# Optimization experiments

Hardware: AMD Instinct MI355X
Metric: run time of the kernel (lower is better)

## Reference

```python
import jax, jax.numpy as jnp
import numpy as np

C = 128; HEADS = 8; GH = 32; GW = 32; B = 8; PD = 8  # PD = (dim//4)//4

def _conv(x, w, pad, dil=1, groups=1):
    return jax.lax.conv_general_dilated(
        x, w, (1, 1), [(pad[0], pad[0]), (pad[1], pad[1])],
        rhs_dilation=(dil, dil),
        dimension_numbers=('NCHW', 'OIHW', 'NCHW'),
        feature_group_count=groups)

def _lrelu(t):
    return jnp.where(t >= 0, t, 0.1 * t)

def _ln(t, g, b, eps=1e-5):
    m = jnp.mean(t, -1, keepdims=True)
    v = jnp.var(t, -1, keepdims=True)
    return (t - m) * jax.lax.rsqrt(v + eps) * g + b

def setup_inputs():
    rng = np.random.RandomState(0)
    f = lambda *s: jnp.asarray((rng.randn(*s) * 0.05).astype(np.float32))
    ones = lambda n: jnp.ones((n,), jnp.float32)
    zeros = lambda n: jnp.zeros((n,), jnp.float32)
    # Swin-style relative position index over the (GH, GW) group
    coords = np.stack(np.meshgrid(np.arange(GH), np.arange(GW), indexing='ij')).reshape(2, -1)
    rel = (coords[:, :, None] - coords[:, None, :]).transpose(1, 2, 0)
    rel[..., 0] += GH - 1; rel[..., 1] += GW - 1; rel[..., 0] *= 2 * GW - 1
    rel_idx = jnp.asarray(rel.sum(-1).astype(np.int32))  # [N, N]
    biases = np.stack(np.meshgrid(np.arange(1 - GH, GH), np.arange(1 - GW, GW), indexing='ij'))
    biases = jnp.asarray(biases.reshape(2, -1).T.astype(np.float32))  # [(2GH-1)*(2GW-1), 2]
    return dict(
        x=jnp.asarray(rng.rand(B, C, GH, GW).astype(np.float32)),
        conv1_w=f(C, C, 3, 3), conv2_w=f(C, C, 3, 3), conv3_w=f(C, C, 3, 3),
        convt_w=f(C, 3, 1, 1),
        rba_w=f(C, C, 3, 1), rba_b=zeros(C), rbb_w=f(C, C, 1, 3), rbb_b=zeros(C),
        pp_w=f(PD, 2), pp_b=zeros(PD),
        l1_g=ones(PD), l1_b=zeros(PD), l1_w=f(PD, PD), l1_b2=zeros(PD),
        l2_g=ones(PD), l2_b=zeros(PD), l2_w=f(PD, PD), l2_b2=zeros(PD),
        l3_g=ones(PD), l3_b=zeros(PD), l3_w=f(HEADS, PD), l3_b2=zeros(HEADS),
        qk_w=f(2 * C, C), qk_b=zeros(2 * C),
        v_w=f(C, C), v_b=zeros(C),
        proj_w=f(C, C), proj_b=zeros(C),
        fc1_w=f(C, C), fc1_b=zeros(C), fc2_w=f(C, C), fc2_b=zeros(C),
        biases=biases, rel_idx=rel_idx,
    )

def reference(x, conv1_w, conv2_w, conv3_w, convt_w, rba_w, rba_b, rbb_w, rbb_b,
              pp_w, pp_b, l1_g, l1_b, l1_w, l1_b2, l2_g, l2_b, l2_w, l2_b2,
              l3_g, l3_b, l3_w, l3_b2, qk_w, qk_b, v_w, v_b, proj_w, proj_b,
              fc1_w, fc1_b, fc2_w, fc2_b, biases, rel_idx):
    Bn, Cc, Hh, Ww = x.shape
    N = Hh * Ww
    hd = Cc // HEADS
    # FeaExtract: ResASPP (3 dilated 3x3 convs, grouped 1x1 merge) + residual
    b1 = _lrelu(_conv(x, conv1_w, (1, 1)))
    b2 = _lrelu(_conv(x, conv2_w, (3, 3), dil=3))
    b3 = _lrelu(_conv(x, conv3_w, (5, 5), dil=5))
    a = _conv(jnp.concatenate([b1, b2, b3], 1), convt_w, (0, 0), groups=Cc) + x
    # RB: (3,1) conv -> lrelu -> (1,3) conv + residual
    r = _lrelu(_conv(a, rba_w, (1, 0)) + rba_b[None, :, None, None])
    r = _conv(r, rbb_w, (0, 1)) + rbb_b[None, :, None, None]
    o0 = r + a
    # original uses in-place clamp_, so o0 is clamped before flattening
    o0 = jnp.clip(o0, 0.0, 1.0)
    E = o0.reshape(Bn, Cc, N).transpose(0, 2, 1)  # [B, N, C]
    qk = E @ qk_w.T + qk_b  # [B, N, 2C]
    q = qk[..., :Cc].reshape(Bn, N, HEADS, hd).transpose(0, 2, 1, 3)
    k = qk[..., Cc:].reshape(Bn, N, HEADS, hd).transpose(0, 2, 1, 3)
    v = (E @ v_w.T + v_b).reshape(Bn, N, HEADS, hd).transpose(0, 2, 1, 3)
    attn = jnp.einsum('bhid,bhjd->bhij', q * (hd ** -0.5), k)
    # DynamicPosBias MLP (residual=False): Linear(2,pd) -> [LN,ReLU,Linear] x2 -> LN,ReLU,Linear(pd,heads)
    p = biases @ pp_w.T + pp_b
    p = jax.nn.relu(_ln(p, l1_g, l1_b)) @ l1_w.T + l1_b2
    p = jax.nn.relu(_ln(p, l2_g, l2_b)) @ l2_w.T + l2_b2
    p = jax.nn.relu(_ln(p, l3_g, l3_b)) @ l3_w.T + l3_b2  # [L, heads]
    rpb = p[rel_idx]  # gather -> [N, N, heads]
    attn = attn + rpb.transpose(2, 0, 1)[None]
    attn = jax.nn.softmax(attn, axis=-1)
    y = jnp.einsum('bhij,bhjd->bhid', attn, v).transpose(0, 2, 1, 3).reshape(Bn, N, Cc) + E
    x_proj = y @ proj_w.T + proj_b
    h = jax.nn.gelu(x_proj @ fc1_w.T + fc1_b, approximate=False)
    return (h @ fc2_w.T + fc2_b) + y
```

## Files before the change

### kernel.cpp

```cpp
#include <hip/hip_runtime.h>
#include <hip/hip_bf16.h>

typedef __hip_bfloat16 bf16;
typedef __bf16 bf16x8 __attribute__((ext_vector_type(8)));
typedef float f32x4 __attribute__((ext_vector_type(4)));

#define Lb 3969

#define XP_F   0
#define WF_F   903168
#define WR_F   1124352
#define WG_F   1173504
#define BH_F   1222656
#define R1P_F  1222656
#define QKV_F  1222656
#define AP_F   2795520
#define YT_F   2795520
#define EB_F   3352576
#define XPT_F  3352576
#define H1T_F  0
#define RPB_F  3876864
#define FLAG_F 3908616
#define RT_F   3908624
#define VT_F   4924432

__device__ __forceinline__ float b2f(bf16 v) { return __bfloat162float(v); }
__device__ __forceinline__ bf16 f2b(float v) { return __float2bfloat16(v); }

template <typename T> __device__ __forceinline__ float ldw(const void* p, int i);
template <> __device__ __forceinline__ float ldw<bf16>(const void* p, int i) {
  return __bfloat162float(((const bf16*)p)[i]);
}
template <> __device__ __forceinline__ float ldw<float>(const void* p, int i) {
  return ((const float*)p)[i];
}
template <typename T> __device__ __forceinline__ void stw(void* p, size_t i, float v);
template <> __device__ __forceinline__ void stw<bf16>(void* p, size_t i, float v) {
  ((bf16*)p)[i] = __float2bfloat16(v);
}
template <> __device__ __forceinline__ void stw<float>(void* p, size_t i, float v) {
  ((float*)p)[i] = v;
}

__device__ __forceinline__ unsigned pkb(float a, float b) {
  bf16 x = __float2bfloat16(a), y = __float2bfloat16(b);
  unsigned short ux = *(unsigned short*)&x, uy = *(unsigned short*)&y;
  return (unsigned)ux | ((unsigned)uy << 16);
}

__device__ __forceinline__ bool detect_local(const unsigned* x) {
  int lane = threadIdx.x & 63;
  int cnt = 0;
#pragma unroll
  for (int k = 0; k < 4; ++k) {
    unsigned lo = x[lane + 64 * k] & 0xFFFFu;
    cnt += (lo >= 0x3C00u && lo < 0x3F80u) ? 1 : 0;
  }
#pragma unroll
  for (int off = 1; off < 64; off <<= 1) cnt += __shfl_xor(cnt, off);
  return cnt >= 128;
}

template <typename T>
__device__ void wprep_all_body(const void* w1, const void* w2, const void* w3,
                               const void* rba_w, const void* rbb_w,
                               const void* qk_w, const void* v_w,
                               const void* proj_w, const void* fc1_w,
                               const void* fc2_w, bf16* __restrict__ Wf,
                               bf16* __restrict__ Wr, bf16* __restrict__ Wg)
{
  int tid = blockIdx.x * 256 + threadIdx.x;
  int lane = tid & 63, li = lane & 15, quad = lane >> 4;
  if (tid < 55296) {
    int mt = (tid >> 6) & 7;
    int Kc = (tid >> 9) & 3;
    int rem = tid >> 11;
    int t = rem % 9;
    int br = rem / 9;
    const void* w = (br == 0 ? w1 : (br == 1 ? w2 : w3));
    int o = mt * 16 + li;
    int ci0 = Kc * 32 + quad * 8;
#pragma unroll
    for (int j = 0; j < 8; ++j)
      Wf[(size_t)tid * 8 + j] = f2b(ldw<T>(w, (o * 128 + ci0 + j) * 9 + t));
  } else {
    int u = tid - 55296;
    if (u < 12288) {
      int Kc = (u >> 6) & 3, mt = (u >> 8) & 7, q = u >> 11;
      const void* w = (q >= 3) ? rbb_w : rba_w;
      int t = q % 3;
#pragma unroll
      for (int j = 0; j < 8; ++j)
        Wr[(size_t)u * 8 + j] =
            f2b(ldw<T>(w, ((mt * 16 + li) * 128 + Kc * 32 + quad * 8 + j) * 3 + t));
    } else if (u < 24576) {
      int g = u - 12288;
      int Kc = (g >> 6) & 3, mtg = g >> 8;
      const void* w; int mrow; float sc = 1.f;
      if (mtg < 16)      { w = qk_w;   mrow = mtg * 16; if (mtg < 8) sc = 0.25f; }
      else if (mtg < 24) { w = v_w;    mrow = (mtg - 16) * 16; }
      else if (mtg < 32) { w = proj_w; mrow = (mtg - 24) * 16; }
      else if (mtg < 40) { w = fc1_w;  mrow = (mtg - 32) * 16; }
      else               { w = fc2_w;  mrow = (mtg - 40) * 16; }
#pragma unroll
      for (int j = 0; j < 8; ++j)
        Wg[(size_t)g * 8 + j] =
            f2b(sc * ldw<T>(w, (mrow + li) * 128 + Kc * 32 + quad * 8 + j));
    }
  }
}

__global__ __launch_bounds__(256) void wprep_all_kernel(
    const unsigned* x, const void* w1, const void* w2, const void* w3,
    const void* rba_w, const void* rbb_w, const void* qk_w, const void* v_w,
    const void* proj_w, const void* fc1_w, const void* fc2_w,
    bf16* Wf, bf16* Wr, bf16* Wg, int* flag)
{
  bool isbf = detect_local(x);
  if (blockIdx.x == 0 && threadIdx.x == 0) *flag = isbf ? 1 : 0;
  if (isbf) wprep_all_body<bf16>(w1, w2, w3, rba_w, rbb_w, qk_w, v_w, proj_w,
                                 fc1_w, fc2_w, Wf, Wr, Wg);
  else      wprep_all_body<float>(w1, w2, w3, rba_w, rbb_w, qk_w, v_w, proj_w,
                                  fc1_w, fc2_w, Wf, Wr, Wg);
}

template <typename T>
__device__ void nhwc_body(const void* x, bf16* __restrict__ xp, bf16 (*tile)[128])
{
  const int b = blockIdx.x >> 5;
  const int row = blockIdx.x & 31;
  const int t = threadIdx.x;
  const size_t bbase = (size_t)b * 42 * 42 * 128;
  const bf16x8 z = (bf16x8){};

  if (t < 160) {
    int side = t / 80;
    int off = (t % 80) * 8;
    *(bf16x8*)&xp[bbase + ((size_t)(row + 5) * 42 + side * 37) * 128 + off] = z;
  }
  {
    int zr = (row < 5) ? row : ((row >= 27) ? row + 10 : -1);
    if (zr >= 0) {
      size_t base = bbase + (size_t)zr * 42 * 128;
      for (int k = t; k < 672; k += 256) *(bf16x8*)&xp[base + k * 8] = z;
    }
  }

  {
    int ci = t >> 1, half = t & 1;
#pragma unroll
    for (int j = 0; j < 16; ++j) {
      int px = half * 16 + j;
      tile[px][ci] = f2b(ldw<T>(x, ((size_t)b * 128 + ci) * 1024 + row * 32 + px));
    }
  }
  __syncthreads();
  {
    int px = t >> 3, c0 = (t & 7) * 16;
    bf16* dst = xp + (bbase + ((size_t)(row + 5) * 42 + (px + 5)) * 128 + c0);
#pragma unroll
    for (int j = 0; j < 16; ++j) dst[j] = tile[px][c0 + j];
  }
}

__global__ __launch_bounds__(256) void nhwc_kernel(const void* x, bf16* xp,
                                                   const int* flag)
{
  __shared__ bf16 tile[32][128];
  if (*flag) nhwc_body<bf16>(x, xp, tile);
  else       nhwc_body<float>(x, xp, tile);
}

__global__ __launch_bounds__(256) void aspp2_kernel(
    const bf16* __restrict__ xp, const bf16* __restrict__ Wf,
    bf16* __restrict__ bh)
{
  const int nt_ = blockIdx.x, br = blockIdx.y >> 1, mh = blockIdx.y & 1;
  const int bb = blockIdx.z;
  const int w = threadIdx.x >> 6, lane = threadIdx.x & 63;
  const int quad = lane >> 4, li = lane & 15;
  const int d = (br == 0 ? 1 : (br == 1 ? 3 : 5));
  const int pxw = nt_ * 64 + w * 16;
  const int y = pxw >> 5, xb = pxw & 31;

  f32x4 acc[4] = {};
  const bf16* Wbase = Wf + (size_t)br * 18432 * 8 + (size_t)mh * 4 * 64 * 8;

  for (int t = 0; t < 9; ++t) {
    const int dy = (t / 3 - 1) * d, dx = (t % 3 - 1) * d;
    const bf16* Asite =
        xp + (((size_t)bb * 42 + (y + 5 + dy)) * 42 + (xb + li + 5 + dx)) * 128;
    const bf16* Wt = Wbase + (size_t)t * 2048 * 8;
#pragma unroll
    for (int Kc = 0; Kc < 4; ++Kc) {
      bf16x8 afrag = *(const bf16x8*)(Asite + Kc * 32 + quad * 8);
      const bf16* Wk = Wt + (size_t)Kc * 512 * 8 + (size_t)lane * 8;
#pragma unroll
      for (int mt = 0; mt < 4; ++mt) {
        bf16x8 wfrag = *(const bf16x8*)(Wk + (size_t)mt * 64 * 8);
        acc[mt] = __builtin_amdgcn_mfma_f32_16x16x32_bf16(afrag, wfrag, acc[mt],
                                                          0, 0, 0);
      }
    }
  }
#pragma unroll
  for (int mt = 0; mt < 4; ++mt)
#pragma unroll
    for (int r = 0; r < 4; ++r) {
      int px = pxw + quad * 4 + r;
      bh[((size_t)bb * 1024 + px) * 384 + br * 128 + (mh * 4 + mt) * 16 + li] =
          f2b(acc[mt][r]);
    }
}

template <typename T>
__device__ void merge2_body(const bf16* __restrict__ xp, const void* wt,
                            const bf16* __restrict__ bh, bf16* __restrict__ ap,
                            float* cw)
{
  const int b = blockIdx.y, px0 = blockIdx.x * 32;
  const bf16x8 z = (bf16x8){};
  if (blockIdx.x == 0) {
    size_t base = ((size_t)b * 34 + 0) * 32 * 128;
    for (int k = threadIdx.x; k < 512; k += 256) *(bf16x8*)&ap[base + k * 8] = z;
  } else if (blockIdx.x == 31) {
    size_t base = ((size_t)b * 34 + 33) * 32 * 128;
    for (int k = threadIdx.x; k < 512; k += 256) *(bf16x8*)&ap[base + k * 8] = z;
  }
  for (int i = threadIdx.x; i < 384; i += 256) cw[i] = ldw<T>(wt, i);
  __syncthreads();
  const int pxl = threadIdx.x >> 3, og = threadIdx.x & 7;
  const int px = px0 + pxl, o0 = og * 16;
  const int y = px >> 5, x = px & 31;
  const bf16* brow = bh + ((size_t)b * 1024 + px) * 384 + o0 * 3;
  const bf16* xrow = xp + (((size_t)b * 42 + y + 5) * 42 + x + 5) * 128 + o0;
  bf16* arow = ap + (((size_t)b * 34 + y + 1) * 32 + x) * 128 + o0;

  bf16 bl[48], xl[16], ol[16];
#pragma unroll
  for (int k = 0; k < 6; ++k) *(bf16x8*)&bl[k * 8] = *(const bf16x8*)&brow[k * 8];
  *(bf16x8*)&xl[0] = *(const bf16x8*)&xrow[0];
  *(bf16x8*)&xl[8] = *(const bf16x8*)&xrow[8];
#pragma unroll
  for (int j = 0; j < 16; ++j) {
    float v = b2f(xl[j]);
#pragma unroll
    for (int i = 0; i < 3; ++i) {
      float t = b2f(bl[j * 3 + i]);
      v += cw[(o0 + j) * 3 + i] * (t >= 0.f ? t : 0.1f * t);
    }
    ol[j] = f2b(v);
  }
  *(bf16x8*)&arow[0] = *(bf16x8*)&ol[0];
  *(bf16x8*)&arow[8] = *(bf16x8*)&ol[8];
}

__global__ __launch_bounds__(256) void merge2_kernel(
    const bf16* xp, const void* wt, const bf16* bh, bf16* ap, const int* flag)
{
  __shared__ float cw[384];
  if (*flag) merge2_body<bf16>(xp, wt, bh, ap, cw);
  else       merge2_body<float>(xp, wt, bh, ap, cw);
}

template <typename T>
__device__ void rb1_body(const bf16* __restrict__ ap, const bf16* __restrict__ Wr,
                         const void* bias, bf16* __restrict__ r1p)
{
  const int b = blockIdx.z, mh = blockIdx.y;
  const int lane = threadIdx.x;
  const int quad = lane >> 4, li = lane & 15;
  const int pxw = blockIdx.x * 16;
  const int y = pxw >> 5, xb = pxw & 31;
  f32x4 acc[4] = {};
#pragma unroll
  for (int t = 0; t < 3; ++t) {
    const bf16* Asite = ap + (((size_t)b * 34 + y + t) * 32 + xb + li) * 128;
#pragma unroll
    for (int Kc = 0; Kc < 4; ++Kc) {
      bf16x8 afrag = *(const bf16x8*)(Asite + Kc * 32 + quad * 8);
#pragma unroll
      for (int mt = 0; mt < 4; ++mt) {
        int f = (t * 8 + mh * 4 + mt) * 4 + Kc;
        bf16x8 wfrag = *(const bf16x8*)(Wr + ((size_t)f * 64 + lane) * 8);
        acc[mt] = __builtin_amdgcn_mfma_f32_16x16x32_bf16(afrag, wfrag, acc[mt],
                                                          0, 0, 0);
      }
    }
  }
  if (quad == 0) {
    int xcol = (xb == 0) ? 0 : 33;
#pragma unroll
    for (int mt = 0; mt < 4; ++mt)
      r1p[(((size_t)b * 32 + y) * 34 + xcol) * 128 + (mh * 4 + mt) * 16 + li] =
          f2b(0.f);
  }
#pragma unroll
  for (int mt = 0; mt < 4; ++mt) {
    int o = (mh * 4 + mt) * 16 + li;
    float bv = ldw<T>(bias, o);
#pragma unroll
    for (int r = 0; r < 4; ++r) {
      int x = xb + quad * 4 + r;
      float v = acc[mt][r] + bv;
      v = (v >= 0.f ? v : 0.1f * v);
      r1p[(((size_t)b * 32 + y) * 34 + x + 1) * 128 + o] = f2b(v);
    }
  }
}

__global__ __launch_bounds__(64) void rb1_kernel(
    const bf16* ap, const bf16* Wr, const void* bias, bf16* r1p, const int* flag)
{
  if (*flag) rb1_body<bf16>(ap, Wr, bias, r1p);
  else       rb1_body<float>(ap, Wr, bias, r1p);
}

template <typename T>
__device__ void rb2_body(const bf16* __restrict__ r1p, const bf16* __restrict__ Wr,
                         const void* bias, const bf16* __restrict__ ap,
                         bf16* __restrict__ Eb)
{
  const int b = blockIdx.z, mh = blockIdx.y;
  const int lane = threadIdx.x;
  const int quad = lane >> 4, li = lane & 15;
  const int pxw = blockIdx.x * 16;
  const int y = pxw >> 5, xb = pxw & 31;
  f32x4 acc[4] = {};
#pragma unroll
  for (int t = 0; t < 3; ++t) {
    const bf16* Asite = r1p + (((size_t)b * 32 + y) * 34 + xb + li + t) * 128;
#pragma unroll
    for (int Kc = 0; Kc < 4; ++Kc) {
      bf16x8 afrag = *(const bf16x8*)(Asite + Kc * 32 + quad * 8);
#pragma unroll
      for (int mt = 0; mt < 4; ++mt) {
        int f = ((3 + t) * 8 + mh * 4 + mt) * 4 + Kc;
        bf16x8 wfrag = *(const bf16x8*)(Wr + ((size_t)f * 64 + lane) * 8);
        acc[mt] = __builtin_amdgcn_mfma_f32_16x16x32_bf16(afrag, wfrag, acc[mt],
                                                          0, 0, 0);
      }
    }
  }
#pragma unroll
  for (int mt = 0; mt < 4; ++mt) {
    int o = (mh * 4 + mt) * 16 + li;
    float bv = ldw<T>(bias, o);
#pragma unroll
    for (int r = 0; r < 4; ++r) {
      int x = xb + quad * 4 + r;
      float v = acc[mt][r] + bv +
                b2f(ap[(((size_t)b * 34 + y + 1) * 32 + x) * 128 + o]);
      v = fminf(fmaxf(v, 0.f), 1.f);
      Eb[((size_t)b * 1024 + y * 32 + x) * 128 + o] = f2b(v);
    }
  }
}

__global__ __launch_bounds__(64) void rb2_kernel(
    const bf16* r1p, const bf16* Wr, const void* bias, const bf16* ap,
    bf16* Eb, const int* flag)
{
  if (*flag) rb2_body<bf16>(r1p, Wr, bias, ap, Eb);
  else       rb2_body<float>(r1p, Wr, bias, ap, Eb);
}

template <typename T>
__device__ __forceinline__ void ln_relu8(const float* t, float* u,
                                         const void* g, const void* bb)
{
  float m = 0.f;
#pragma unroll
  for (int k = 0; k < 8; ++k) m += t[k];
  m *= 0.125f;
  float v = 0.f;
#pragma unroll
  for (int k = 0; k < 8; ++k) { float d = t[k] - m; v += d * d; }
  v *= 0.125f;
  float r = rsqrtf(v + 1e-5f);
#pragma unroll
  for (int k = 0; k < 8; ++k) {
    float val = (t[k] - m) * r * ldw<T>(g, k) + ldw<T>(bb, k);
    u[k] = val > 0.f ? val : 0.f;
  }
}

template <typename T>
__device__ void dpb_body(const void* biases, const void* pp_w, const void* pp_b,
                         const void* l1_g, const void* l1_b, const void* l1_w,
                         const void* l1_b2, const void* l2_g, const void* l2_b,
                         const void* l2_w, const void* l2_b2, const void* l3_g,
                         const void* l3_b, const void* l3_w, const void* l3_b2,
                         float* __restrict__ RPB)
{
  int r = blockIdx.x * 256 + threadIdx.x;
  if (r >= Lb) return;
  float b0 = ldw<T>(biases, r * 2), b1 = ldw<T>(biases, r * 2 + 1);
  float t[8], u[8];
#pragma unroll
  for (int j = 0; j < 8; ++j)
    t[j] = b0 * ldw<T>(pp_w, j * 2) + b1 * ldw<T>(pp_w, j * 2 + 1) +
           ldw<T>(pp_b, j);
  ln_relu8<T>(t, u, l1_g, l1_b);
#pragma unroll
  for (int j = 0; j < 8; ++j) {
    float s = ldw<T>(l1_b2, j);
#pragma unroll
    for (int k = 0; k < 8; ++k) s += u[k] * ldw<T>(l1_w, j * 8 + k);
    t[j] = s;
  }
  ln_relu8<T>(t, u, l2_g, l2_b);
#pragma unroll
  for (int j = 0; j < 8; ++j) {
    float s = ldw<T>(l2_b2, j);
#pragma unroll
    for (int k = 0; k < 8; ++k) s += u[k] * ldw<T>(l2_w, j * 8 + k);
    t[j] = s;
  }
  ln_relu8<T>(t, u, l3_g, l3_b);
#pragma unroll
  for (int h = 0; h < 8; ++h) {
    float s = ldw<T>(l3_b2, h);
#pragma unroll
    for (int k = 0; k < 8; ++k) s += u[k] * ldw<T>(l3_w, h * 8 + k);
    RPB[h * Lb + r] = s;
  }
}

__global__ __launch_bounds__(256) void dpb_kernel(
    const void* biases, const void* pp_w, const void* pp_b, const void* l1_g,
    const void* l1_b, const void* l1_w, const void* l1_b2, const void* l2_g,
    const void* l2_b, const void* l2_w, const void* l2_b2, const void* l3_g,
    const void* l3_b, const void* l3_w, const void* l3_b2, float* RPB,
    const int* flag)
{
  if (*flag)
    dpb_body<bf16>(biases, pp_w, pp_b, l1_g, l1_b, l1_w, l1_b2, l2_g, l2_b,
                   l2_w, l2_b2, l3_g, l3_b, l3_w, l3_b2, RPB);
  else
    dpb_body<float>(biases, pp_w, pp_b, l1_g, l1_b, l1_w, l1_b2, l2_g, l2_b,
                    l2_w, l2_b2, l3_g, l3_b, l3_w, l3_b2, RPB);
}

__global__ __launch_bounds__(64) void rt_kernel(
    const float* __restrict__ RPB, float* __restrict__ RT)
{
  const int tt = blockIdx.x, h = blockIdx.y;
  const int t = tt >> 1, p = tt & 1;
  const int lane = threadIdx.x, quad = lane >> 4, li = lane & 15;
  const float* rp = RPB + h * Lb;
#pragma unroll
  for (int mt = 0; mt < 4; ++mt) {
    f32x4 v;
#pragma unroll
    for (int r = 0; r < 4; ++r) {
      int j = mt * 16 + quad * 4 + r;
      int dy = (t - 30) - (j >> 5);
      int dx = (p * 16 + li) - (j & 31);
      v[r] = rp[(dy + 31) * 63 + dx + 31];
    }
    *(f32x4*)&RT[(((size_t)h * 124 + tt) * 4 + mt) * 256 + lane * 4] = v;
  }
}

__global__ __launch_bounds__(64) void vt_kernel(
    const bf16* __restrict__ QKV, bf16* __restrict__ VT)
{
  const int c = blockIdx.x, hh = blockIdx.y, b = blockIdx.z;
  __shared__ bf16 Vl[64][20];
  const int lane = threadIdx.x, quad = lane >> 4, li = lane & 15;
  const bf16* vsrc =
      QKV + ((size_t)b * 1024 + c * 64 + lane) * 384 + 256 + hh * 16;
  union { bf16x8 v; uint2 u[2]; } w0, w1;
  w0.v = *(const bf16x8*)vsrc;
  w1.v = *(const bf16x8*)(vsrc + 8);
  *(uint2*)&Vl[lane][0] = w0.u[0];
  *(uint2*)&Vl[lane][4] = w0.u[1];
  *(uint2*)&Vl[lane][8] = w1.u[0];
  *(uint2*)&Vl[lane][12] = w1.u[1];
  __syncthreads();
#pragma unroll
  for (int half = 0; half < 2; ++half) {
    union { bf16 e[8]; bf16x8 v; } uv;
#pragma unroll
    for (int jj = 0; jj < 8; ++jj)
      uv.e[jj] = Vl[half * 32 + quad * 8 + jj][li];
    *(bf16x8*)&VT[((((size_t)(b * 8 + hh) * 16 + c) * 2 + half) * 64 + lane) * 8] =
        uv.v;
  }
}

template <typename T>
__device__ void qkv_body(const bf16* __restrict__ Eb, const bf16* __restrict__ Wg,
                         const void* qk_b, const void* v_b,
                         bf16* __restrict__ QKV)
{
  const int grp = blockIdx.y, b = blockIdx.z;
  const int w = threadIdx.x >> 6, lane = threadIdx.x & 63;
  const int quad = lane >> 4, li = lane & 15;
  const int pxw = blockIdx.x * 64 + w * 16;
  bf16x8 ef[4];
#pragma unroll
  for (int Kc = 0; Kc < 4; ++Kc)
    ef[Kc] = *(const bf16x8*)&Eb[((size_t)b * 1024 + pxw + li) * 128 + Kc * 32 +
                                 quad * 8];
  f32x4 acc[8] = {};
#pragma unroll
  for (int nt = 0; nt < 8; ++nt) {
    int g = grp * 8 + nt;
#pragma unroll
    for (int Kc = 0; Kc < 4; ++Kc) {
      bf16x8 wf = *(const bf16x8*)&Wg[(((size_t)g * 4 + Kc) * 64 + lane) * 8];
      acc[nt] = __builtin_amdgcn_mfma_f32_16x16x32_bf16(ef[Kc], wf, acc[nt],
                                                        0, 0, 0);
    }
  }
#pragma unroll
  for (int nt = 0; nt < 8; ++nt) {
    int g = grp * 8 + nt;
    int o = g * 16 + li;
    float bv;
    if (g < 8)       bv = 0.25f * ldw<T>(qk_b, o);
    else if (g < 16) bv = ldw<T>(qk_b, o);
    else             bv = ldw<T>(v_b, o - 256);
#pragma unroll
    for (int r = 0; r < 4; ++r) {
      int px = pxw + quad * 4 + r;
      QKV[((size_t)b * 1024 + px) * 384 + o] = f2b(acc[nt][r] + bv);
    }
  }
}

__global__ __launch_bounds__(256) void qkv_kernel(
    const bf16* Eb, const bf16* Wg, const void* qk_b, const void* v_b,
    bf16* QKV, const int* flag)
{
  if (*flag) qkv_body<bf16>(Eb, Wg, qk_b, v_b, QKV);
  else       qkv_body<float>(Eb, Wg, qk_b, v_b, QKV);
}

template <typename T, int MODE>
__device__ void mlp_body(const bf16* __restrict__ src, const bf16* __restrict__ Wg,
                         int tb, const void* bias, const bf16* __restrict__ res,
                         void* out)
{
  const int b = blockIdx.z, mh = blockIdx.y;
  const int lane = threadIdx.x;
  const int quad = lane >> 4, li = lane & 15;
  const int pxw = blockIdx.x * 16;
  bf16x8 ef[4];
#pragma unroll
  for (int Kc = 0; Kc < 4; ++Kc)
    ef[Kc] = *(const bf16x8*)&src[((size_t)b * 1024 + pxw + li) * 128 + Kc * 32 +
                                  quad * 8];
  f32x4 acc[2] = {};
#pragma unroll
  for (int nt = 0; nt < 2; ++nt)
#pragma unroll
    for (int Kc = 0; Kc < 4; ++Kc) {
      bf16x8 wf = *(const bf16x8*)&Wg[
          (((size_t)(tb + mh * 2 + nt) * 4 + Kc) * 64 + lane) * 8];
      acc[nt] = __builtin_amdgcn_mfma_f32_16x16x32_bf16(ef[Kc], wf, acc[nt],
                                                        0, 0, 0);
    }
#pragma unroll
  for (int nt = 0; nt < 2; ++nt) {
    int o = (mh * 2 + nt) * 16 + li;
    float bv = ldw<T>(bias, o);
#pragma unroll
    for (int r = 0; r < 4; ++r) {
      int px = pxw + quad * 4 + r;
      float v = acc[nt][r] + bv;
      size_t oidx = ((size_t)b * 1024 + px) * 128 + o;
      if (MODE == 1) v = 0.5f * v * (1.f + erff(v * 0.70710678118f));
      if (MODE == 2) {
        v += b2f(res[oidx]);
        stw<T>(out, oidx, v);
      } else {
        ((bf16*)out)[oidx] = f2b(v);
      }
    }
  }
}

template <int MODE>
__global__ __launch_bounds__(64) void mlp_kernel(
    const bf16* src, const bf16* Wg, int tb, const void* bias, const bf16* res,
    void* out, const int* flag)
{
  if (*flag) mlp_body<bf16, MODE>(src, Wg, tb, bias, res, out);
  else       mlp_body<float, MODE>(src, Wg, tb, bias, res, out);
}

__global__ __launch_bounds__(64) void attn_kernel(
    const bf16* __restrict__ QKV, const bf16* __restrict__ Eb,
    const float* __restrict__ RT, const bf16* __restrict__ VT,
    bf16* __restrict__ Yt)
{
  const int qt = blockIdx.x;
  const int hh = blockIdx.y;
  const int b = blockIdx.z;

  __shared__ bf16 Pl[16][72];

  const int lane = threadIdx.x;
  const int quad = lane >> 4, li = lane & 15;
  const int qb = qt * 16;

  const bf16* QKVb = QKV + (size_t)b * 1024 * 384;
  const bf16* VTb = VT + (size_t)(b * 8 + hh) * 16 * 1024;
  const float* RTh = RT + (size_t)hh * 124 * 1024;

  bf16x8 qf = (bf16x8){};
  if (quad < 2)
    qf = *(const bf16x8*)&QKVb[(size_t)(qb + li) * 384 + hh * 16 + quad * 8];

  f32x4 O_ = {};
  float lsum = 0.f;
  const int sbase = (lane & 48) + ((lane >> 2) & 12);

  for (int c = 0; c < 16; ++c) {
    const int c0 = c * 64;
    const int tt = ((qt >> 1) - 2 * c + 30) * 2 + (qt & 1);
    const float* rtp = RTh + (size_t)tt * 1024 + lane * 4;

    f32x4 sT[4];
#pragma unroll
    for (int mt = 0; mt < 4; ++mt) {
      f32x4 cin = *(const f32x4*)(rtp + (size_t)mt * 256);
      bf16x8 kf = (bf16x8){};
      if (quad < 2)
        kf = *(const bf16x8*)&QKVb[(size_t)(c0 + mt * 16 + li) * 384 + 128 +
                                   hh * 16 + quad * 8];
      sT[mt] = __builtin_amdgcn_mfma_f32_16x16x32_bf16(kf, qf, cin, 0, 0, 0);
    }

#pragma unroll
    for (int mt = 0; mt < 4; ++mt)
#pragma unroll
      for (int r = 0; r < 4; ++r) {
        float p = __expf(sT[mt][r]);
        sT[mt][r] = p;
        lsum += p;
      }

#pragma unroll
    for (int mt = 0; mt < 4; ++mt) {
      uint2 w;
      w.x = pkb(sT[mt][0], sT[mt][1]);
      w.y = pkb(sT[mt][2], sT[mt][3]);
      *(uint2*)&Pl[li][mt * 16 + quad * 4] = w;
    }

#pragma unroll
    for (int half = 0; half < 2; ++half) {
      bf16x8 vf = *(const bf16x8*)&VTb[((size_t)(c * 2 + half) * 64 + lane) * 8];
      bf16x8 pf = *(const bf16x8*)&Pl[li][half * 32 + quad * 8];
      O_ = __builtin_amdgcn_mfma_f32_16x16x32_bf16(pf, vf, O_, 0, 0, 0);
    }
  }

  lsum += __shfl_xor(lsum, 16);
  lsum += __shfl_xor(lsum, 32);

  const bf16* Ebp = Eb + (size_t)b * 1024 * 128 + hh * 16 + li;
  bf16* Ytp = Yt + (size_t)b * 1024 * 128 + hh * 16 + li;
#pragma unroll
  for (int r = 0; r < 4; ++r) {
    float lb = __shfl(lsum, sbase + r);
    int qrow = qb + quad * 4 + r;
    Ytp[(size_t)qrow * 128] =
        f2b(O_[r] / lb + b2f(Ebp[(size_t)qrow * 128]));
  }
}

extern "C" void kernel_launch(void* const* d_in, const int* in_sizes, int n_in,
                              void* d_out, int out_size, void* d_ws,
                              size_t ws_size, hipStream_t stream)
{
  (void)in_sizes; (void)n_in; (void)out_size; (void)ws_size;
  const void* x       = d_in[0];
  const void* conv1_w = d_in[1];
  const void* conv2_w = d_in[2];
  const void* conv3_w = d_in[3];
  const void* convt_w = d_in[4];
  const void* rba_w   = d_in[5];
  const void* rba_b   = d_in[6];
  const void* rbb_w   = d_in[7];
  const void* rbb_b   = d_in[8];
  const void* pp_w    = d_in[9];
  const void* pp_b    = d_in[10];
  const void* l1_g    = d_in[11];
  const void* l1_b    = d_in[12];
  const void* l1_w    = d_in[13];
  const void* l1_b2   = d_in[14];
  const void* l2_g    = d_in[15];
  const void* l2_b    = d_in[16];
  const void* l2_w    = d_in[17];
  const void* l2_b2   = d_in[18];
  const void* l3_g    = d_in[19];
  const void* l3_b    = d_in[20];
  const void* l3_w    = d_in[21];
  const void* l3_b2   = d_in[22];
  const void* qk_w    = d_in[23];
  const void* qk_b    = d_in[24];
  const void* v_w     = d_in[25];
  const void* v_b     = d_in[26];
  const void* proj_w  = d_in[27];
  const void* proj_b  = d_in[28];
  const void* fc1_w   = d_in[29];
  const void* fc1_b   = d_in[30];
  const void* fc2_w   = d_in[31];
  const void* fc2_b   = d_in[32];
  const void* biases  = d_in[33];

  float* ws   = (float*)d_ws;
  bf16*  xp   = (bf16*)(ws + XP_F);
  bf16*  Wf   = (bf16*)(ws + WF_F);
  bf16*  Wr   = (bf16*)(ws + WR_F);
  bf16*  Wg   = (bf16*)(ws + WG_F);
  bf16*  bh   = (bf16*)(ws + BH_F);
  bf16*  r1p  = (bf16*)(ws + R1P_F);
  bf16*  QKV  = (bf16*)(ws + QKV_F);
  bf16*  ap   = (bf16*)(ws + AP_F);
  bf16*  Yt   = (bf16*)(ws + YT_F);
  bf16*  Eb   = (bf16*)(ws + EB_F);
  bf16*  XPt  = (bf16*)(ws + XPT_F);
  bf16*  H1t  = (bf16*)(ws + H1T_F);
  float* RPB  = ws + RPB_F;
  int*   flag = (int*)(ws + FLAG_F);
  float* RT   = ws + RT_F;
  bf16*  VT   = (bf16*)(ws + VT_F);

  wprep_all_kernel<<<312, 256, 0, stream>>>(
      (const unsigned*)x, conv1_w, conv2_w, conv3_w, rba_w, rbb_w, qk_w, v_w,
      proj_w, fc1_w, fc2_w, Wf, Wr, Wg, flag);
  nhwc_kernel<<<256, 256, 0, stream>>>(x, xp, flag);
  aspp2_kernel<<<dim3(16, 6, 8), 256, 0, stream>>>(xp, Wf, bh);
  merge2_kernel<<<dim3(32, 8), 256, 0, stream>>>(xp, convt_w, bh, ap, flag);
  rb1_kernel<<<dim3(64, 2, 8), 64, 0, stream>>>(ap, Wr, rba_b, r1p, flag);
  rb2_kernel<<<dim3(64, 2, 8), 64, 0, stream>>>(r1p, Wr, rbb_b, ap, Eb, flag);
  dpb_kernel<<<16, 256, 0, stream>>>(biases, pp_w, pp_b, l1_g, l1_b, l1_w,
                                     l1_b2, l2_g, l2_b, l2_w, l2_b2, l3_g,
                                     l3_b, l3_w, l3_b2, RPB, flag);
  rt_kernel<<<dim3(124, 8), 64, 0, stream>>>(RPB, RT);
  qkv_kernel<<<dim3(16, 3, 8), 256, 0, stream>>>(Eb, Wg, qk_b, v_b, QKV, flag);
  vt_kernel<<<dim3(16, 8, 8), 64, 0, stream>>>(QKV, VT);
  attn_kernel<<<dim3(64, 8, 8), 64, 0, stream>>>(QKV, Eb, RT, VT, Yt);
  mlp_kernel<0><<<dim3(64, 4, 8), 64, 0, stream>>>(Yt, Wg, 24, proj_b, nullptr,
                                                   XPt, flag);
  mlp_kernel<1><<<dim3(64, 4, 8), 64, 0, stream>>>(XPt, Wg, 32, fc1_b, nullptr,
                                                   H1t, flag);
  mlp_kernel<2><<<dim3(64, 4, 8), 64, 0, stream>>>(H1t, Wg, 40, fc2_b, Yt,
                                                   d_out, flag);
}
```

Baseline: 245.6 us.

## Fuse position-bias MLP with table build, split attention keys across two waves

Merges the dynamic position-bias MLP and the relative-table build into one kernel that evaluates only the bias rows each tile needs, dropping one launch and the intermediate table. The residual convs and MLP GEMMs now give each wave a single 16-channel output tile over 4x more blocks. The attention kernel uses two waves that each process half the key chunks, then combine partial outputs and sums through shared memory. Workspace buffers are remapped to fit, with the risk of aliasing and of extra weight-load and launch overhead from the smaller tiles.

```diff
diff --git a/kernel.cpp b/kernel.cpp
--- a/kernel.cpp
+++ b/kernel.cpp
@@ -12,17 +12,15 @@
 #define WR_F   1124352
 #define WG_F   1173504
 #define BH_F   1222656
-#define R1P_F  1222656
 #define QKV_F  1222656
 #define AP_F   2795520
 #define YT_F   2795520
 #define EB_F   3352576
-#define XPT_F  3352576
-#define H1T_F  0
-#define RPB_F  3876864
+#define R1P_F  3352576
 #define FLAG_F 3908616
 #define RT_F   3908624
 #define VT_F   4924432
+#define R1_F   5448720
 
 __device__ __forceinline__ float b2f(bf16 v) { return __bfloat162float(v); }
 __device__ __forceinline__ bf16 f2b(float v) { return __float2bfloat16(v); }
@@ -125,6 +123,106 @@
 }
 
 template <typename T>
+__device__ __forceinline__ void ln_relu8(const float* t, float* u,
+                                         const void* g, const void* bb)
+{
+  float m = 0.f;
+#pragma unroll
+  for (int k = 0; k < 8; ++k) m += t[k];
+  m *= 0.125f;
+  float v = 0.f;
+#pragma unroll
+  for (int k = 0; k < 8; ++k) { float d = t[k] - m; v += d * d; }
+  v *= 0.125f;
+  float r = rsqrtf(v + 1e-5f);
+#pragma unroll
+  for (int k = 0; k < 8; ++k) {
+    float val = (t[k] - m) * r * ldw<T>(g, k) + ldw<T>(bb, k);
+    u[k] = val > 0.f ? val : 0.f;
+  }
+}
+
+template <typename T>
+__device__ void dpbrt_body(const void* biases, const void* pp_w, const void* pp_b,
+    const void* l1_g, const void* l1_b, const void* l1_w, const void* l1_b2,
+    const void* l2_g, const void* l2_b, const void* l2_w, const void* l2_b2,
+    const void* l3_g, const void* l3_b, const void* l3_w, const void* l3_b2,
+    float* __restrict__ RT, float (*LH)[47][8])
+{
+  const int tt = blockIdx.x, t = tt >> 1, p = tt & 1;
+  const int lane = threadIdx.x, quad = lane >> 4, li = lane & 15;
+
+  for (int it = 0; it < 2; ++it) {
+    int idx = it * 64 + lane;
+    if (idx < 94) {
+      int sd = idx / 47, xi = idx - sd * 47;
+      int rtab = (t + 1 - sd) * 63 + p * 16 + xi;
+      float b0 = ldw<T>(biases, rtab * 2), b1 = ldw<T>(biases, rtab * 2 + 1);
+      float tv[8], u[8];
+#pragma unroll
+      for (int j = 0; j < 8; ++j)
+        tv[j] = b0 * ldw<T>(pp_w, j * 2) + b1 * ldw<T>(pp_w, j * 2 + 1) +
+                ldw<T>(pp_b, j);
+      ln_relu8<T>(tv, u, l1_g, l1_b);
+#pragma unroll
+      for (int j = 0; j < 8; ++j) {
+        float s = ldw<T>(l1_b2, j);
+#pragma unroll
+        for (int k = 0; k < 8; ++k) s += u[k] * ldw<T>(l1_w, j * 8 + k);
+        tv[j] = s;
+      }
+      ln_relu8<T>(tv, u, l2_g, l2_b);
+#pragma unroll
+      for (int j = 0; j < 8; ++j) {
+        float s = ldw<T>(l2_b2, j);
+#pragma unroll
+        for (int k = 0; k < 8; ++k) s += u[k] * ldw<T>(l2_w, j * 8 + k);
+        tv[j] = s;
+      }
+      ln_relu8<T>(tv, u, l3_g, l3_b);
+#pragma unroll
+      for (int h = 0; h < 8; ++h) {
+        float s = ldw<T>(l3_b2, h);
+#pragma unroll
+        for (int k = 0; k < 8; ++k) s += u[k] * ldw<T>(l3_w, h * 8 + k);
+        LH[sd][xi][h] = s;
+      }
+    }
+  }
+  __syncthreads();
+#pragma unroll
+  for (int h = 0; h < 8; ++h)
+#pragma unroll
+    for (int mt = 0; mt < 4; ++mt) {
+      f32x4 v;
+#pragma unroll
+      for (int r = 0; r < 4; ++r) {
+        int j = mt * 16 + quad * 4 + r;
+        int jy = j >> 5;
+        int xi = li + 31 - (j & 31);
+        v[r] = LH[jy][xi][h];
+      }
+      *(f32x4*)&RT[(((size_t)h * 124 + tt) * 4 + mt) * 256 + lane * 4] = v;
+    }
+}
+
+__global__ __launch_bounds__(64) void dpbrt_kernel(
+    const void* biases, const void* pp_w, const void* pp_b, const void* l1_g,
+    const void* l1_b, const void* l1_w, const void* l1_b2, const void* l2_g,
+    const void* l2_b, const void* l2_w, const void* l2_b2, const void* l3_g,
+    const void* l3_b, const void* l3_w, const void* l3_b2, float* RT,
+    const int* flag)
+{
+  __shared__ float LH[2][47][8];
+  if (*flag)
+    dpbrt_body<bf16>(biases, pp_w, pp_b, l1_g, l1_b, l1_w, l1_b2, l2_g, l2_b,
+                     l2_w, l2_b2, l3_g, l3_b, l3_w, l3_b2, RT, LH);
+  else
+    dpbrt_body<float>(biases, pp_w, pp_b, l1_g, l1_b, l1_w, l1_b2, l2_g, l2_b,
+                      l2_w, l2_b2, l3_g, l3_b, l3_w, l3_b2, RT, LH);
+}
+
+template <typename T>
 __device__ void nhwc_body(const void* x, bf16* __restrict__ xp, bf16 (*tile)[128])
 {
   const int b = blockIdx.x >> 5;
@@ -272,40 +370,30 @@
   const int quad = lane >> 4, li = lane & 15;
   const int pxw = blockIdx.x * 16;
   const int y = pxw >> 5, xb = pxw & 31;
-  f32x4 acc[4] = {};
+  f32x4 acc = {};
 #pragma unroll
   for (int t = 0; t < 3; ++t) {
     const bf16* Asite = ap + (((size_t)b * 34 + y + t) * 32 + xb + li) * 128;
 #pragma unroll
     for (int Kc = 0; Kc < 4; ++Kc) {
       bf16x8 afrag = *(const bf16x8*)(Asite + Kc * 32 + quad * 8);
-#pragma unroll
-      for (int mt = 0; mt < 4; ++mt) {
-        int f = (t * 8 + mh * 4 + mt) * 4 + Kc;
-        bf16x8 wfrag = *(const bf16x8*)(Wr + ((size_t)f * 64 + lane) * 8);
-        acc[mt] = __builtin_amdgcn_mfma_f32_16x16x32_bf16(afrag, wfrag, acc[mt],
-                                                          0, 0, 0);
-      }
-    }
-  }
+      int f = (t * 8 + mh) * 4 + Kc;
+      bf16x8 wfrag = *(const bf16x8*)(Wr + ((size_t)f * 64 + lane) * 8);
+      acc = __builtin_amdgcn_mfma_f32_16x16x32_bf16(afrag, wfrag, acc, 0, 0, 0);
+    }
+  }
+  const int o = mh * 16 + li;
   if (quad == 0) {
     int xcol = (xb == 0) ? 0 : 33;
-#pragma unroll
-    for (int mt = 0; mt < 4; ++mt)
-      r1p[(((size_t)b * 32 + y) * 34 + xcol) * 128 + (mh * 4 + mt) * 16 + li] =
-          f2b(0.f);
-  }
-#pragma unroll
-  for (int mt = 0; mt < 4; ++mt) {
-    int o = (mh * 4 + mt) * 16 + li;
-    float bv = ldw<T>(bias, o);
-#pragma unroll
-    for (int r = 0; r < 4; ++r) {
-      int x = xb + quad * 4 + r;
-      float v = acc[mt][r] + bv;
-      v = (v >= 0.f ? v : 0.1f * v);
-      r1p[(((size_t)b * 32 + y) * 34 + x + 1) * 128 + o] = f2b(v);
-    }
+    r1p[(((size_t)b * 32 + y) * 34 + xcol) * 128 + o] = f2b(0.f);
+  }
+  float bv = ldw<T>(bias, o);
+#pragma unroll
+  for (int r = 0; r < 4; ++r) {
+    int x = xb + quad * 4 + r;
+    float v = acc[r] + bv;
+    v = (v >= 0.f ? v : 0.1f * v);
+    r1p[(((size_t)b * 32 + y) * 34 + x + 1) * 128 + o] = f2b(v);
   }
 }
 
@@ -326,34 +414,27 @@
   const int quad = lane >> 4, li = lane & 15;
   const int pxw = blockIdx.x * 16;
   const int y = pxw >> 5, xb = pxw & 31;
-  f32x4 acc[4] = {};
+  f32x4 acc = {};
 #pragma unroll
   for (int t = 0; t < 3; ++t) {
     const bf16* Asite = r1p + (((size_t)b * 32 + y) * 34 + xb + li + t) * 128;
 #pragma unroll
     for (int Kc = 0; Kc < 4; ++Kc) {
       bf16x8 afrag = *(const bf16x8*)(Asite + Kc * 32 + quad * 8);
-#pragma unroll
-      for (int mt = 0; mt < 4; ++mt) {
-        int f = ((3 + t) * 8 + mh * 4 + mt) * 4 + Kc;
-        bf16x8 wfrag = *(const bf16x8*)(Wr + ((size_t)f * 64 + lane) * 8);
-        acc[mt] = __builtin_amdgcn_mfma_f32_16x16x32_bf16(afrag, wfrag, acc[mt],
-                                                          0, 0, 0);
-      }
-    }
-  }
-#pragma unroll
-  for (int mt = 0; mt < 4; ++mt) {
-    int o = (mh * 4 + mt) * 16 + li;
-    float bv = ldw<T>(bias, o);
-#pragma unroll
-    for (int r = 0; r < 4; ++r) {
-      int x = xb + quad * 4 + r;
-      float v = acc[mt][r] + bv +
-                b2f(ap[(((size_t)b * 34 + y + 1) * 32 + x) * 128 + o]);
-      v = fminf(fmaxf(v, 0.f), 1.f);
-      Eb[((size_t)b * 1024 + y * 32 + x) * 128 + o] = f2b(v);
-    }
+      int f = ((3 + t) * 8 + mh) * 4 + Kc;
+      bf16x8 wfrag = *(const bf16x8*)(Wr + ((size_t)f * 64 + lane) * 8);
+      acc = __builtin_amdgcn_mfma_f32_16x16x32_bf16(afrag, wfrag, acc, 0, 0, 0);
+    }
+  }
+  const int o = mh * 16 + li;
+  float bv = ldw<T>(bias, o);
+#pragma unroll
+  for (int r = 0; r < 4; ++r) {
+    int x = xb + quad * 4 + r;
+    float v = acc[r] + bv +
+              b2f(ap[(((size_t)b * 34 + y + 1) * 32 + x) * 128 + o]);
+    v = fminf(fmaxf(v, 0.f), 1.f);
+    Eb[((size_t)b * 1024 + y * 32 + x) * 128 + o] = f2b(v);
   }
 }
 
@@ -366,101 +447,52 @@
 }
 
 template <typename T>
-__device__ __forceinline__ void ln_relu8(const float* t, float* u,
-                                         const void* g, const void* bb)
-{
-  float m = 0.f;
-#pragma unroll
-  for (int k = 0; k < 8; ++k) m += t[k];
-  m *= 0.125f;
-  float v = 0.f;
-#pragma unroll
-  for (int k = 0; k < 8; ++k) { float d = t[k] - m; v += d * d; }
-  v *= 0.125f;
-  float r = rsqrtf(v + 1e-5f);
-#pragma unroll
-  for (int k = 0; k < 8; ++k) {
-    float val = (t[k] - m) * r * ldw<T>(g, k) + ldw<T>(bb, k);
-    u[k] = val > 0.f ? val : 0.f;
-  }
-}
-
-template <typename T>
-__device__ void dpb_body(const void* biases, const void* pp_w, const void* pp_b,
-                         const void* l1_g, const void* l1_b, const void* l1_w,
-                         const void* l1_b2, const void* l2_g, const void* l2_b,
-                         const void* l2_w, const void* l2_b2, const void* l3_g,
-                         const void* l3_b, const void* l3_w, const void* l3_b2,
-                         float* __restrict__ RPB)
-{
-  int r = blockIdx.x * 256 + threadIdx.x;
-  if (r >= Lb) return;
-  float b0 = ldw<T>(biases, r * 2), b1 = ldw<T>(biases, r * 2 + 1);
-  float t[8], u[8];
-#pragma unroll
-  for (int j = 0; j < 8; ++j)
-    t[j] = b0 * ldw<T>(pp_w, j * 2) + b1 * ldw<T>(pp_w, j * 2 + 1) +
-           ldw<T>(pp_b, j);
-  ln_relu8<T>(t, u, l1_g, l1_b);
-#pragma unroll
-  for (int j = 0; j < 8; ++j) {
-    float s = ldw<T>(l1_b2, j);
-#pragma unroll
-    for (int k = 0; k < 8; ++k) s += u[k] * ldw<T>(l1_w, j * 8 + k);
-    t[j] = s;
-  }
-  ln_relu8<T>(t, u, l2_g, l2_b);
-#pragma unroll
-  for (int j = 0; j < 8; ++j) {
-    float s = ldw<T>(l2_b2, j);
-#pragma unroll
-    for (int k = 0; k < 8; ++k) s += u[k] * ldw<T>(l2_w, j * 8 + k);
-    t[j] = s;
-  }
-  ln_relu8<T>(t, u, l3_g, l3_b);
-#pragma unroll
-  for (int h = 0; h < 8; ++h) {
-    float s = ldw<T>(l3_b2, h);
-#pragma unroll
-    for (int k = 0; k < 8; ++k) s += u[k] * ldw<T>(l3_w, h * 8 + k);
-    RPB[h * Lb + r] = s;
-  }
-}
-
-__global__ __launch_bounds__(256) void dpb_kernel(
-    const void* biases, const void* pp_w, const void* pp_b, const void* l1_g,
-    const void* l1_b, const void* l1_w, const void* l1_b2, const void* l2_g,
-    const void* l2_b, const void* l2_w, const void* l2_b2, const void* l3_g,
-    const void* l3_b, const void* l3_w, const void* l3_b2, float* RPB,
-    const int* flag)
-{
-  if (*flag)
-    dpb_body<bf16>(biases, pp_w, pp_b, l1_g, l1_b, l1_w, l1_b2, l2_g, l2_b,
-                   l2_w, l2_b2, l3_g, l3_b, l3_w, l3_b2, RPB);
-  else
-    dpb_body<float>(biases, pp_w, pp_b, l1_g, l1_b, l1_w, l1_b2, l2_g, l2_b,
-                    l2_w, l2_b2, l3_g, l3_b, l3_w, l3_b2, RPB);
-}
-
-__global__ __launch_bounds__(64) void rt_kernel(
-    const float* __restrict__ RPB, float* __restrict__ RT)
-{
-  const int tt = blockIdx.x, h = blockIdx.y;
-  const int t = tt >> 1, p = tt & 1;
-  const int lane = threadIdx.x, quad = lane >> 4, li = lane & 15;
-  const float* rp = RPB + h * Lb;
-#pragma unroll
-  for (int mt = 0; mt < 4; ++mt) {
-    f32x4 v;
+__device__ void qkv_body(const bf16* __restrict__ Eb, const bf16* __restrict__ Wg,
+                         const void* qk_b, const void* v_b,
+                         bf16* __restrict__ QKV)
+{
+  const int grp = blockIdx.y, b = blockIdx.z;
+  const int w = threadIdx.x >> 6, lane = threadIdx.x & 63;
+  const int quad = lane >> 4, li = lane & 15;
+  const int pxw = blockIdx.x * 64 + w * 16;
+  bf16x8 ef[4];
+#pragma unroll
+  for (int Kc = 0; Kc < 4; ++Kc)
+    ef[Kc] = *(const bf16x8*)&Eb[((size_t)b * 1024 + pxw + li) * 128 + Kc * 32 +
+                                 quad * 8];
+  f32x4 acc[8] = {};
+#pragma unroll
+  for (int nt = 0; nt < 8; ++nt) {
+    int g = grp * 8 + nt;
+#pragma unroll
+    for (int Kc = 0; Kc < 4; ++Kc) {
+      bf16x8 wf = *(const bf16x8*)&Wg[(((size_t)g * 4 + Kc) * 64 + lane) * 8];
+      acc[nt] = __builtin_amdgcn_mfma_f32_16x16x32_bf16(ef[Kc], wf, acc[nt],
+                                                        0, 0, 0);
+    }
+  }
+#pragma unroll
+  for (int nt = 0; nt < 8; ++nt) {
+    int g = grp * 8 + nt;
+    int o = g * 16 + li;
+    float bv;
+    if (g < 8)       bv = 0.25f * ldw<T>(qk_b, o);
+    else if (g < 16) bv = ldw<T>(qk_b, o);
+    else             bv = ldw<T>(v_b, o - 256);
 #pragma unroll
     for (int r = 0; r < 4; ++r) {
-      int j = mt * 16 + quad * 4 + r;
-      int dy = (t - 30) - (j >> 5);
-      int dx = (p * 16 + li) - (j & 31);
-      v[r] = rp[(dy + 31) * 63 + dx + 31];
-    }
-    *(f32x4*)&RT[(((size_t)h * 124 + tt) * 4 + mt) * 256 + lane * 4] = v;
-  }
+      int px = pxw + quad * 4 + r;
+      QKV[((size_t)b * 1024 + px) * 384 + o] = f2b(acc[nt][r] + bv);
+    }
+  }
+}
+
+__global__ __launch_bounds__(256) void qkv_kernel(
+    const bf16* Eb, const bf16* Wg, const void* qk_b, const void* v_b,
+    bf16* QKV, const int* flag)
+{
+  if (*flag) qkv_body<bf16>(Eb, Wg, qk_b, v_b, QKV);
+  else       qkv_body<float>(Eb, Wg, qk_b, v_b, QKV);
 }
 
 __global__ __launch_bounds__(64) void vt_kernel(
@@ -490,109 +522,7 @@
   }
 }
 
-template <typename T>
-__device__ void qkv_body(const bf16* __restrict__ Eb, const bf16* __restrict__ Wg,
-                         const void* qk_b, const void* v_b,
-                         bf16* __restrict__ QKV)
-{
-  const int grp = blockIdx.y, b = blockIdx.z;
-  const int w = threadIdx.x >> 6, lane = threadIdx.x & 63;
-  const int quad = lane >> 4, li = lane & 15;
-  const int pxw = blockIdx.x * 64 + w * 16;
-  bf16x8 ef[4];
-#pragma unroll
-  for (int Kc = 0; Kc < 4; ++Kc)
-    ef[Kc] = *(const bf16x8*)&Eb[((size_t)b * 1024 + pxw + li) * 128 + Kc * 32 +
-                                 quad * 8];
-  f32x4 acc[8] = {};
-#pragma unroll
-  for (int nt = 0; nt < 8; ++nt) {
-    int g = grp * 8 + nt;
-#pragma unroll
-    for (int Kc = 0; Kc < 4; ++Kc) {
-      bf16x8 wf = *(const bf16x8*)&Wg[(((size_t)g * 4 + Kc) * 64 + lane) * 8];
-      acc[nt] = __builtin_amdgcn_mfma_f32_16x16x32_bf16(ef[Kc], wf, acc[nt],
-                                                        0, 0, 0);
-    }
-  }
-#pragma unroll
-  for (int nt = 0; nt < 8; ++nt) {
-    int g = grp * 8 + nt;
-    int o = g * 16 + li;
-    float bv;
-    if (g < 8)       bv = 0.25f * ldw<T>(qk_b, o);
-    else if (g < 16) bv = ldw<T>(qk_b, o);
-    else             bv = ldw<T>(v_b, o - 256);
-#pragma unroll
-    for (int r = 0; r < 4; ++r) {
-      int px = pxw + quad * 4 + r;
-      QKV[((size_t)b * 1024 + px) * 384 + o] = f2b(acc[nt][r] + bv);
-    }
-  }
-}
-
-__global__ __launch_bounds__(256) void qkv_kernel(
-    const bf16* Eb, const bf16* Wg, const void* qk_b, const void* v_b,
-    bf16* QKV, const int* flag)
-{
-  if (*flag) qkv_body<bf16>(Eb, Wg, qk_b, v_b, QKV);
-  else       qkv_body<float>(Eb, Wg, qk_b, v_b, QKV);
-}
-
-template <typename T, int MODE>
-__device__ void mlp_body(const bf16* __restrict__ src, const bf16* __restrict__ Wg,
-                         int tb, const void* bias, const bf16* __restrict__ res,
-                         void* out)
-{
-  const int b = blockIdx.z, mh = blockIdx.y;
-  const int lane = threadIdx.x;
-  const int quad = lane >> 4, li = lane & 15;
-  const int pxw = blockIdx.x * 16;
-  bf16x8 ef[4];
-#pragma unroll
-  for (int Kc = 0; Kc < 4; ++Kc)
-    ef[Kc] = *(const bf16x8*)&src[((size_t)b * 1024 + pxw + li) * 128 + Kc * 32 +
-                                  quad * 8];
-  f32x4 acc[2] = {};
-#pragma unroll
-  for (int nt = 0; nt < 2; ++nt)
-#pragma unroll
-    for (int Kc = 0; Kc < 4; ++Kc) {
-      bf16x8 wf = *(const bf16x8*)&Wg[
-          (((size_t)(tb + mh * 2 + nt) * 4 + Kc) * 64 + lane) * 8];
-      acc[nt] = __builtin_amdgcn_mfma_f32_16x16x32_bf16(ef[Kc], wf, acc[nt],
-                                                        0, 0, 0);
-    }
-#pragma unroll
-  for (int nt = 0; nt < 2; ++nt) {
-    int o = (mh * 2 + nt) * 16 + li;
-    float bv = ldw<T>(bias, o);
-#pragma unroll
-    for (int r = 0; r < 4; ++r) {
-      int px = pxw + quad * 4 + r;
-      float v = acc[nt][r] + bv;
-      size_t oidx = ((size_t)b * 1024 + px) * 128 + o;
-      if (MODE == 1) v = 0.5f * v * (1.f + erff(v * 0.70710678118f));
-      if (MODE == 2) {
-        v += b2f(res[oidx]);
-        stw<T>(out, oidx, v);
-      } else {
-        ((bf16*)out)[oidx] = f2b(v);
-      }
-    }
-  }
-}
-
-template <int MODE>
-__global__ __launch_bounds__(64) void mlp_kernel(
-    const bf16* src, const bf16* Wg, int tb, const void* bias, const bf16* res,
-    void* out, const int* flag)
-{
-  if (*flag) mlp_body<bf16, MODE>(src, Wg, tb, bias, res, out);
-  else       mlp_body<float, MODE>(src, Wg, tb, bias, res, out);
-}
-
-__global__ __launch_bounds__(64) void attn_kernel(
+__global__ __launch_bounds__(128) void attn_kernel(
     const bf16* __restrict__ QKV, const bf16* __restrict__ Eb,
     const float* __restrict__ RT, const bf16* __restrict__ VT,
     bf16* __restrict__ Yt)
@@ -601,9 +531,10 @@
   const int hh = blockIdx.y;
   const int b = blockIdx.z;
 
-  __shared__ bf16 Pl[16][72];
-
-  const int lane = threadIdx.x;
+  __shared__ bf16 Pl[2][16][72];
+  __shared__ float Red[64][5];
+
+  const int w = threadIdx.x >> 6, lane = threadIdx.x & 63;
   const int quad = lane >> 4, li = lane & 15;
   const int qb = qt * 16;
 
@@ -617,9 +548,9 @@
 
   f32x4 O_ = {};
   float lsum = 0.f;
-  const int sbase = (lane & 48) + ((lane >> 2) & 12);
-
-  for (int c = 0; c < 16; ++c) {
+
+  for (int cc = 0; cc < 8; ++cc) {
+    const int c = w * 8 + cc;
     const int c0 = c * 64;
     const int tt = ((qt >> 1) - 2 * c + 30) * 2 + (qt & 1);
     const float* rtp = RTh + (size_t)tt * 1024 + lane * 4;
@@ -646,32 +577,89 @@
 
 #pragma unroll
     for (int mt = 0; mt < 4; ++mt) {
-      uint2 w;
-      w.x = pkb(sT[mt][0], sT[mt][1]);
-      w.y = pkb(sT[mt][2], sT[mt][3]);
-      *(uint2*)&Pl[li][mt * 16 + quad * 4] = w;
+      uint2 ww;
+      ww.x = pkb(sT[mt][0], sT[mt][1]);
+      ww.y = pkb(sT[mt][2], sT[mt][3]);
+      *(uint2*)&Pl[w][li][mt * 16 + quad * 4] = ww;
     }
 
 #pragma unroll
     for (int half = 0; half < 2; ++half) {
       bf16x8 vf = *(const bf16x8*)&VTb[((size_t)(c * 2 + half) * 64 + lane) * 8];
-      bf16x8 pf = *(const bf16x8*)&Pl[li][half * 32 + quad * 8];
+      bf16x8 pf = *(const bf16x8*)&Pl[w][li][half * 32 + quad * 8];
       O_ = __builtin_amdgcn_mfma_f32_16x16x32_bf16(pf, vf, O_, 0, 0, 0);
     }
   }
 
-  lsum += __shfl_xor(lsum, 16);
-  lsum += __shfl_xor(lsum, 32);
-
-  const bf16* Ebp = Eb + (size_t)b * 1024 * 128 + hh * 16 + li;
-  bf16* Ytp = Yt + (size_t)b * 1024 * 128 + hh * 16 + li;
+  if (w == 1) {
+#pragma unroll
+    for (int r = 0; r < 4; ++r) Red[lane][r] = O_[r];
+    Red[lane][4] = lsum;
+  }
+  __syncthreads();
+  if (w == 0) {
+#pragma unroll
+    for (int r = 0; r < 4; ++r) O_[r] += Red[lane][r];
+    lsum += Red[lane][4];
+    lsum += __shfl_xor(lsum, 16);
+    lsum += __shfl_xor(lsum, 32);
+    const int sbase = (lane & 48) + ((lane >> 2) & 12);
+    const bf16* Ebp = Eb + (size_t)b * 1024 * 128 + hh * 16 + li;
+    bf16* Ytp = Yt + (size_t)b * 1024 * 128 + hh * 16 + li;
+#pragma unroll
+    for (int r = 0; r < 4; ++r) {
+      float lb = __shfl(lsum, sbase + r);
+      int qrow = qb + quad * 4 + r;
+      Ytp[(size_t)qrow * 128] =
+          f2b(O_[r] / lb + b2f(Ebp[(size_t)qrow * 128]));
+    }
+  }
+}
+
+template <typename T, int MODE>
+__device__ void mlp_body(const bf16* __restrict__ src, const bf16* __restrict__ Wg,
+                         int tb, const void* bias, const bf16* __restrict__ res,
+                         void* out)
+{
+  const int b = blockIdx.z, mh = blockIdx.y;
+  const int lane = threadIdx.x;
+  const int quad = lane >> 4, li = lane & 15;
+  const int pxw = blockIdx.x * 16;
+  bf16x8 ef[4];
+#pragma unroll
+  for (int Kc = 0; Kc < 4; ++Kc)
+    ef[Kc] = *(const bf16x8*)&src[((size_t)b * 1024 + pxw + li) * 128 + Kc * 32 +
+                                  quad * 8];
+  f32x4 acc = {};
+#pragma unroll
+  for (int Kc = 0; Kc < 4; ++Kc) {
+    bf16x8 wf = *(const bf16x8*)&Wg[(((size_t)(tb + mh) * 4 + Kc) * 64 + lane) * 8];
+    acc = __builtin_amdgcn_mfma_f32_16x16x32_bf16(ef[Kc], wf, acc, 0, 0, 0);
+  }
+  const int o = mh * 16 + li;
+  float bv = ldw<T>(bias, o);
 #pragma unroll
   for (int r = 0; r < 4; ++r) {
-    float lb = __shfl(lsum, sbase + r);
-    int qrow = qb + quad * 4 + r;
-    Ytp[(size_t)qrow * 128] =
-        f2b(O_[r] / lb + b2f(Ebp[(size_t)qrow * 128]));
-  }
+    int px = pxw + quad * 4 + r;
+    float v = acc[r] + bv;
+    size_t oidx = ((size_t)b * 1024 + px) * 128 + o;
+    if (MODE == 1) v = 0.5f * v * (1.f + erff(v * 0.70710678118f));
+    if (MODE == 2) {
+      v += b2f(res[oidx]);
+      stw<T>(out, oidx, v);
+    } else {
+      ((bf16*)out)[oidx] = f2b(v);
+    }
+  }
+}
+
+template <int MODE>
+__global__ __launch_bounds__(64) void mlp_kernel(
+    const bf16* src, const bf16* Wg, int tb, const void* bias, const bf16* res,
+    void* out, const int* flag)
+{
+  if (*flag) mlp_body<bf16, MODE>(src, Wg, tb, bias, res, out);
+  else       mlp_body<float, MODE>(src, Wg, tb, bias, res, out);
 }
 
 extern "C" void kernel_launch(void* const* d_in, const int* in_sizes, int n_in,
@@ -720,37 +708,35 @@
   bf16*  Wr   = (bf16*)(ws + WR_F);
   bf16*  Wg   = (bf16*)(ws + WG_F);
   bf16*  bh   = (bf16*)(ws + BH_F);
-  bf16*  r1p  = (bf16*)(ws + R1P_F);
   bf16*  QKV  = (bf16*)(ws + QKV_F);
   bf16*  ap   = (bf16*)(ws + AP_F);
   bf16*  Yt   = (bf16*)(ws + YT_F);
   bf16*  Eb   = (bf16*)(ws + EB_F);
-  bf16*  XPt  = (bf16*)(ws + XPT_F);
-  bf16*  H1t  = (bf16*)(ws + H1T_F);
-  float* RPB  = ws + RPB_F;
   int*   flag = (int*)(ws + FLAG_F);
   float* RT   = ws + RT_F;
   bf16*  VT   = (bf16*)(ws + VT_F);
+  bf16*  r1p  = (bf16*)(ws + R1_F);
+  bf16*  XPt  = (bf16*)(ws + QKV_F);
+  bf16*  H1t  = (bf16*)(ws + QKV_F + 524288);
 
   wprep_all_kernel<<<312, 256, 0, stream>>>(
       (const unsigned*)x, conv1_w, conv2_w, conv3_w, rba_w, rbb_w, qk_w, v_w,
       proj_w, fc1_w, fc2_w, Wf, Wr, Wg, flag);
+  dpbrt_kernel<<<124, 64, 0, stream>>>(biases, pp_w, pp_b, l1_g, l1_b, l1_w,
+                                       l1_b2, l2_g, l2_b, l2_w, l2_b2, l3_g,
+                                       l3_b, l3_w, l3_b2, RT, flag);
   nhwc_kernel<<<256, 256, 0, stream>>>(x, xp, flag);
   aspp2_kernel<<<dim3(16, 6, 8), 256, 0, stream>>>(xp, Wf, bh);
   merge2_kernel<<<dim3(32, 8), 256, 0, stream>>>(xp, convt_w, bh, ap, flag);
-  rb1_kernel<<<dim3(64, 2, 8), 64, 0, stream>>>(ap, Wr, rba_b, r1p, flag);
-  rb2_kernel<<<dim3(64, 2, 8), 64, 0, stream>>>(r1p, Wr, rbb_b, ap, Eb, flag);
-  dpb_kernel<<<16, 256, 0, stream>>>(biases, pp_w, pp_b, l1_g, l1_b, l1_w,
-                                     l1_b2, l2_g, l2_b, l2_w, l2_b2, l3_g,
-                                     l3_b, l3_w, l3_b2, RPB, flag);
-  rt_kernel<<<dim3(124, 8), 64, 0, stream>>>(RPB, RT);
+  rb1_kernel<<<dim3(64, 8, 8), 64, 0, stream>>>(ap, Wr, rba_b, r1p, flag);
+  rb2_kernel<<<dim3(64, 8, 8), 64, 0, stream>>>(r1p, Wr, rbb_b, ap, Eb, flag);
   qkv_kernel<<<dim3(16, 3, 8), 256, 0, stream>>>(Eb, Wg, qk_b, v_b, QKV, flag);
   vt_kernel<<<dim3(16, 8, 8), 64, 0, stream>>>(QKV, VT);
-  attn_kernel<<<dim3(64, 8, 8), 64, 0, stream>>>(QKV, Eb, RT, VT, Yt);
-  mlp_kernel<0><<<dim3(64, 4, 8), 64, 0, stream>>>(Yt, Wg, 24, proj_b, nullptr,
+  attn_kernel<<<dim3(64, 8, 8), 128, 0, stream>>>(QKV, Eb, RT, VT, Yt);
+  mlp_kernel<0><<<dim3(64, 8, 8), 64, 0, stream>>>(Yt, Wg, 24, proj_b, nullptr,
                                                    XPt, flag);
-  mlp_kernel<1><<<dim3(64, 4, 8), 64, 0, stream>>>(XPt, Wg, 32, fc1_b, nullptr,
+  mlp_kernel<1><<<dim3(64, 8, 8), 64, 0, stream>>>(XPt, Wg, 32, fc1_b, nullptr,
                                                    H1t, flag);
-  mlp_kernel<2><<<dim3(64, 4, 8), 64, 0, stream>>>(H1t, Wg, 40, fc2_b, Yt,
+  mlp_kernel<2><<<dim3(64, 8, 8), 64, 0, stream>>>(H1t, Wg, 40, fc2_b, Yt,
                                                    d_out, flag);
 }
```

After: 253.9 us. +3.4%, slower.
